# Kernel optimization log

Hardware: AMD Instinct MI355X
Metric: run time of the kernel (lower is better)

The kernel has to match this reference:

```python
import jax, jax.numpy as jnp
import numpy as np

E, H, F, T = 8, 2048, 4096, 16384  # experts, hidden, ffn, total tokens


def setup_inputs() -> dict:
    key = jax.random.key(0)
    k1, k2, k3 = jax.random.split(key, 3)
    std = 1.0 / np.sqrt(H)
    x = jax.random.normal(k1, (T, H), dtype=jnp.float32)
    # trunc_normal_(std=std) ~ normal * std for reference purposes
    w_gate_up = jax.random.normal(k2, (E, 2 * F, H), dtype=jnp.float32) * std
    w_down = jax.random.normal(k3, (E, H, F), dtype=jnp.float32) * std
    # tokens are pre-sorted by expert; uniform routing: T//E tokens per expert
    tokens_per_expert = jnp.full((E,), T // E, dtype=jnp.int64)
    return {"x": x, "w_gate_up": w_gate_up, "w_down": w_down,
            "tokens_per_expert": tokens_per_expert}


def reference(x, w_gate_up, w_down, tokens_per_expert):
    # x: [T, H] sorted by expert; uniform tokens_per_expert => grouped GEMM
    # is a batched GEMM over the expert axis (same math as the per-expert
    # sequential fallback: gate_up = xi @ w_gate_up[i].T, etc.).
    e = w_gate_up.shape[0]
    f = w_down.shape[2]
    xe = x.reshape(e, -1, x.shape[-1])                     # [E, T/E, H]
    gate_up = jnp.einsum('eth,efh->etf', xe, w_gate_up)    # [E, T/E, 2F]
    gate, up = gate_up[..., :f], gate_up[..., f:]
    hidden = jax.nn.silu(gate) * up                        # [E, T/E, F]
    out = jnp.einsum('etf,ehf->eth', hidden, w_down)       # [E, T/E, H]
    return out.reshape(x.shape)
```

## Files before the change

kernel.cpp:

```cpp
#include <hip/hip_runtime.h>
#include <stdint.h>

typedef unsigned short u16;
typedef unsigned int u32;
typedef short bf16x8 __attribute__((ext_vector_type(8)));
typedef float f32x4 __attribute__((ext_vector_type(4)));

#define E_ 8
#define H_ 2048
#define F_ 4096
#define T_ 16384
#define TE_ 2048

#define WAITV(n) asm volatile("s_waitcnt vmcnt(" #n ")" ::: "memory")
#define BARF                       \
  do {                             \
    asm volatile("" ::: "memory"); \
    __builtin_amdgcn_s_barrier();  \
    asm volatile("" ::: "memory"); \
  } while (0)

__device__ __forceinline__ u16 f2bf(float f) {
  u32 u = __builtin_bit_cast(u32, f);
  u32 r = (u + 0x7FFFu + ((u >> 16) & 1u)) >> 16;
  return (u16)r;
}

__device__ __forceinline__ void gload16(const u16* g, u16* l) {
  __builtin_amdgcn_global_load_lds(
      (__attribute__((address_space(1))) void*)g,
      (__attribute__((address_space(3))) void*)l, 16, 0, 0);
}

__device__ __forceinline__ void mfma_b(f32x4& acc, bf16x8 a, bf16x8 b) {
  asm volatile("v_mfma_f32_16x16x32_bf16 %0, %1, %2, %0"
               : "+v"(acc)
               : "v"(a), "v"(b));
}


__global__ __launch_bounds__(256) void cvt3_kernel(
    const float* __restrict__ s0, const float* __restrict__ s1,
    const float* __restrict__ s2, u16* __restrict__ dst, long n0, long n1,
    long n2) {
  long i = (long)blockIdx.x * blockDim.x + threadIdx.x;
  long stride = (long)gridDim.x * blockDim.x;
  const long ntot = n0 + n1 + n2;
  uint2* d4 = (uint2*)dst;
  for (; i < ntot; i += stride) {
    const float4* s4;
    long j;
    if (i < n0) {
      s4 = (const float4*)s0;
      j = i;
    } else if (i < n0 + n1) {
      s4 = (const float4*)s1;
      j = i - n0;
    } else {
      s4 = (const float4*)s2;
      j = i - n0 - n1;
    }
    float4 v = s4[j];
    uint2 o;
    o.x = (u32)f2bf(v.x) | ((u32)f2bf(v.y) << 16);
    o.y = (u32)f2bf(v.z) | ((u32)f2bf(v.w) << 16);
    d4[i] = o;
  }
}


__global__ __launch_bounds__(256, 2) void gemm1_silu(
    const u16* __restrict__ Xb, const u16* __restrict__ Wgu,
    u16* __restrict__ Hid, long sX, long sW, long sH) {
  const int z = blockIdx.z;
  Xb += (long)z * sX;
  Wgu += (long)z * sW;
  Hid += (long)z * sH;

  const int bx = blockIdx.x;
  const int by = blockIdx.y;
  const int tid = threadIdx.x;
  const int w = tid >> 6;
  const int lane = tid & 63;
  const int wr = w >> 1, wc = w & 1;
  const int fr = lane & 15, q = lane >> 4, l7 = lane & 7;

  __shared__ __attribute__((aligned(16))) u16 lds[2 * 16384];

  const int srow8 = lane >> 3;
  const int sgran = (lane & 7) ^ (lane >> 3);
  const u16* gA = Xb + (size_t)(by * 128 + srow8) * H_ + sgran * 8;
  const u16* gBg = Wgu + (size_t)(bx * 64 + srow8) * H_ + sgran * 8;
  const u16* gBu = gBg + (size_t)F_ * H_;

  auto stage = [&](int t, int buf) {
    u16* L = lds + buf * 16384;
    const int ko = t * 64;
#pragma unroll
    for (int i = 0; i < 4; ++i) {
      const int c = i * 4 + w;
      gload16(gA + (size_t)(c * 8) * H_ + ko, L + c * 512 + lane * 8);
    }
#pragma unroll
    for (int i = 0; i < 2; ++i) {
      const int c = i * 4 + w;
      gload16(gBg + (size_t)(c * 8) * H_ + ko, L + 8192 + c * 512 + lane * 8);
      gload16(gBu + (size_t)(c * 8) * H_ + ko, L + 12288 + c * 512 + lane * 8);
    }
  };

  f32x4 accG[4][2] = {};
  f32x4 accU[4][2] = {};

  auto comp = [&](int buf) {
    const u16* L = lds + buf * 16384;
#pragma unroll
    for (int ks = 0; ks < 2; ++ks) {
      const int seg = (((ks << 2) + q) ^ l7) << 3;
      bf16x8 a[4], bg[2], bu[2];
#pragma unroll
      for (int mi = 0; mi < 4; ++mi)
        a[mi] = *(const bf16x8*)&L[(wr * 64 + mi * 16 + fr) * 64 + seg];
#pragma unroll
      for (int ni = 0; ni < 2; ++ni) {
        bg[ni] = *(const bf16x8*)&L[8192 + (wc * 32 + ni * 16 + fr) * 64 + seg];
        bu[ni] =
            *(const bf16x8*)&L[12288 + (wc * 32 + ni * 16 + fr) * 64 + seg];
      }
      __builtin_amdgcn_s_setprio(1);
#pragma unroll
      for (int mi = 0; mi < 4; ++mi)
#pragma unroll
        for (int ni = 0; ni < 2; ++ni) {
          mfma_b(accG[mi][ni], a[mi], bg[ni]);
          mfma_b(accU[mi][ni], a[mi], bu[ni]);
        }
      __builtin_amdgcn_s_setprio(0);
    }
  };

  const int NT = H_ / 64;
  stage(0, 0);
  stage(1, 1);
  for (int t = 0; t < NT - 1; ++t) {
    WAITV(8);
    BARF;
    comp(t & 1);
    BARF;
    if (t + 2 < NT) stage(t + 2, t & 1);
  }
  WAITV(0);
  BARF;
  comp((NT - 1) & 1);

  const int row0 = by * 128 + wr * 64 + q * 4;
  const int col0 = bx * 64 + wc * 32 + fr;
#pragma unroll
  for (int mi = 0; mi < 4; ++mi)
#pragma unroll
    for (int ni = 0; ni < 2; ++ni)
#pragma unroll
      for (int j = 0; j < 4; ++j) {
        float g = accG[mi][ni][j];
        float u = accU[mi][ni][j];
        float h = (g / (1.f + __expf(-g))) * u;
        Hid[(size_t)(row0 + mi * 16 + j) * F_ + col0 + ni * 16] = f2bf(h);
      }
}


__global__ __launch_bounds__(512) void gemm2_down(const u16* __restrict__ Hd,
                                                  const u16* __restrict__ Wd,
                                                  float* __restrict__ Out,
                                                  long sH, long sW, long sO) {
  const int z = blockIdx.z;
  Hd += (long)z * sH;
  Wd += (long)z * sW;
  Out += (long)z * sO;

  const int bx = blockIdx.x;
  const int by = blockIdx.y;
  const int tid = threadIdx.x;
  const int w = tid >> 6;
  const int lane = tid & 63;
  const int wr = w >> 1, wc = w & 1;

  __shared__ __attribute__((aligned(16))) u16 lds[3 * 24576];

  const int srow = (w << 3) + (lane >> 3);
  const int scol = (((lane & 7) ^ (lane >> 3)) << 3);
  const u16* gA = Hd + (size_t)((by << 8) + srow) * F_ + scol;
  const u16* gB = Wd + (size_t)((bx << 7) + srow) * F_ + scol;

  auto stage = [&](int t, int buf) {
    u16* L = &lds[buf * 24576];
    const int ko = t << 6;
    const int wb = w << 3;
#pragma unroll
    for (int i = 0; i < 4; ++i)
      gload16(gA + (size_t)(i * 64) * F_ + ko, &L[((i << 6) + wb) << 6]);
#pragma unroll
    for (int i = 0; i < 2; ++i)
      gload16(gB + (size_t)(i * 64) * F_ + ko,
              &L[16384 + (((i << 6) + wb) << 6)]);
  };

  f32x4 acc[4][4] = {};
  const int fr = lane & 15, q = lane >> 4, l7 = lane & 7;

  auto comp = [&](int buf) {
    const u16* L = &lds[buf * 24576];
    bf16x8 a[4][2], b[4][2];
#pragma unroll
    for (int ni = 0; ni < 4; ++ni)
#pragma unroll
      for (int ks = 0; ks < 2; ++ks) {
        int r = (wc << 6) + (ni << 4) + fr;
        b[ni][ks] =
            *(const bf16x8*)&L[16384 + (r << 6) + ((((ks << 2) + q) ^ l7) << 3)];
      }
#pragma unroll
    for (int mi = 0; mi < 4; ++mi)
#pragma unroll
      for (int ks = 0; ks < 2; ++ks) {
        int r = (wr << 6) + (mi << 4) + fr;
        a[mi][ks] = *(const bf16x8*)&L[(r << 6) + ((((ks << 2) + q) ^ l7) << 3)];
      }
    __builtin_amdgcn_s_setprio(1);
#pragma unroll
    for (int mi = 0; mi < 4; ++mi)
#pragma unroll
      for (int ni = 0; ni < 4; ++ni)
#pragma unroll
        for (int ks = 0; ks < 2; ++ks)
          mfma_b(acc[mi][ni], a[mi][ks], b[ni][ks]);
    __builtin_amdgcn_s_setprio(0);
  };

  const int NT = F_ / 64;
  stage(0, 0);
  stage(1, 1);
  int b0 = 0, b1 = 1, b2 = 2;
  for (int t = 0; t < NT - 2; ++t) {
    stage(t + 2, b2);
    WAITV(12);
    BARF;
    comp(b0);
    BARF;
    int tmp = b0; b0 = b1; b1 = b2; b2 = tmp;
  }
  WAITV(6); BARF;
  comp(b0);
  BARF;
  WAITV(0); BARF;
  comp(b1);

  const int row0 = (by << 8) + (wr << 6) + (q << 2);
  const int col0 = (bx << 7) + (wc << 6) + fr;
#pragma unroll
  for (int mi = 0; mi < 4; ++mi)
#pragma unroll
    for (int ni = 0; ni < 4; ++ni)
#pragma unroll
      for (int j = 0; j < 4; ++j)
        Out[(size_t)(row0 + (mi << 4) + j) * H_ + col0 + (ni << 4)] =
            acc[mi][ni][j];
}


extern "C" void kernel_launch(void* const* d_in, const int* in_sizes, int n_in,
                              void* d_out, int out_size, void* d_ws,
                              size_t ws_size, hipStream_t stream) {
  (void)in_sizes;
  (void)n_in;
  (void)out_size;
  const float* x = (const float*)d_in[0];
  const float* wgu = (const float*)d_in[1];
  const float* wdn = (const float*)d_in[2];
  float* out = (float*)d_out;
  u16* ws = (u16*)d_ws;

  const size_t xbN = (size_t)T_ * H_;
  const size_t wguN = (size_t)E_ * 2 * F_ * H_;
  const size_t wdnN = (size_t)E_ * H_ * F_;
  const size_t hidN = (size_t)T_ * F_;
  const size_t fullBytes = (xbN + wguN + wdnN + hidN) * 2;

  dim3 cblk(256), g1blk(256), g2blk(512);

  if (ws_size >= fullBytes) {
    u16* xb = ws;
    u16* wgub = xb + xbN;
    u16* wdnb = wgub + wguN;
    u16* hid = wdnb + wdnN;
    cvt3_kernel<<<4096, cblk, 0, stream>>>(x, wgu, wdn, ws, (long)(xbN / 4),
                                           (long)(wguN / 4), (long)(wdnN / 4));
    gemm1_silu<<<dim3(F_ / 64, TE_ / 128, E_), g1blk, 0, stream>>>(
        xb, wgub, hid, (long)TE_ * H_, (long)2 * F_ * H_, (long)TE_ * F_);
    gemm2_down<<<dim3(H_ / 128, TE_ / 256, E_), g2blk, 0, stream>>>(
        hid, wdnb, out, (long)TE_ * F_, (long)H_ * F_, (long)TE_ * H_);
  } else {
    u16* xb = ws;
    u16* wgub = xb + (size_t)TE_ * H_;
    u16* wdnb = wgub + (size_t)2 * F_ * H_;
    u16* hid = wdnb + (size_t)H_ * F_;
    for (int e = 0; e < E_; ++e) {
      cvt3_kernel<<<2048, cblk, 0, stream>>>(
          x + (size_t)e * TE_ * H_, wgu + (size_t)e * 2 * F_ * H_,
          wdn + (size_t)e * H_ * F_, ws, (long)((size_t)TE_ * H_ / 4),
          (long)((size_t)2 * F_ * H_ / 4), (long)((size_t)H_ * F_ / 4));
      gemm1_silu<<<dim3(F_ / 64, TE_ / 128, 1), g1blk, 0, stream>>>(xb, wgub,
                                                                    hid, 0, 0,
                                                                    0);
      gemm2_down<<<dim3(H_ / 128, TE_ / 256, 1), g2blk, 0, stream>>>(
          hid, wdnb, out + (size_t)e * TE_ * H_, 0, 0, 0);
    }
  }
}
```

Before: 1.097 ms.

## Retile down-projection GEMM to 128x128 with double buffering; split conversion kernel

New measurement: 1.075 ms, median of 2. Within noise of the previous version (-2.0%).

```diff
diff --git a/kernel.cpp b/kernel.cpp
--- a/kernel.cpp
+++ b/kernel.cpp
@@ -39,28 +39,15 @@
 }
 
 
-__global__ __launch_bounds__(256) void cvt3_kernel(
-    const float* __restrict__ s0, const float* __restrict__ s1,
-    const float* __restrict__ s2, u16* __restrict__ dst, long n0, long n1,
-    long n2) {
+__global__ __launch_bounds__(256) void cvt_kernel(const float* __restrict__ src,
+                                                  u16* __restrict__ dst,
+                                                  long n4) {
   long i = (long)blockIdx.x * blockDim.x + threadIdx.x;
   long stride = (long)gridDim.x * blockDim.x;
-  const long ntot = n0 + n1 + n2;
+  const float4* s4 = (const float4*)src;
   uint2* d4 = (uint2*)dst;
-  for (; i < ntot; i += stride) {
-    const float4* s4;
-    long j;
-    if (i < n0) {
-      s4 = (const float4*)s0;
-      j = i;
-    } else if (i < n0 + n1) {
-      s4 = (const float4*)s1;
-      j = i - n0;
-    } else {
-      s4 = (const float4*)s2;
-      j = i - n0 - n1;
-    }
-    float4 v = s4[j];
+  for (; i < n4; i += stride) {
+    float4 v = s4[i];
     uint2 o;
     o.x = (u32)f2bf(v.x) | ((u32)f2bf(v.y) << 16);
     o.y = (u32)f2bf(v.z) | ((u32)f2bf(v.w) << 16);
@@ -169,10 +156,9 @@
 }
 
 
-__global__ __launch_bounds__(512) void gemm2_down(const u16* __restrict__ Hd,
-                                                  const u16* __restrict__ Wd,
-                                                  float* __restrict__ Out,
-                                                  long sH, long sW, long sO) {
+__global__ __launch_bounds__(256, 2) void gemm2_down(
+    const u16* __restrict__ Hd, const u16* __restrict__ Wd,
+    float* __restrict__ Out, long sH, long sW, long sO) {
   const int z = blockIdx.z;
   Hd += (long)z * sH;
   Wd += (long)z * sW;
@@ -184,86 +170,72 @@
   const int w = tid >> 6;
   const int lane = tid & 63;
   const int wr = w >> 1, wc = w & 1;
-
-  __shared__ __attribute__((aligned(16))) u16 lds[3 * 24576];
-
-  const int srow = (w << 3) + (lane >> 3);
-  const int scol = (((lane & 7) ^ (lane >> 3)) << 3);
-  const u16* gA = Hd + (size_t)((by << 8) + srow) * F_ + scol;
-  const u16* gB = Wd + (size_t)((bx << 7) + srow) * F_ + scol;
+  const int fr = lane & 15, q = lane >> 4, l7 = lane & 7;
+
+  __shared__ __attribute__((aligned(16))) u16 lds[2 * 16384];
+
+  const int srow8 = lane >> 3;
+  const int sgran = (lane & 7) ^ (lane >> 3);
+  const u16* gA = Hd + (size_t)(by * 128 + srow8) * F_ + sgran * 8;
+  const u16* gB = Wd + (size_t)(bx * 128 + srow8) * F_ + sgran * 8;
 
   auto stage = [&](int t, int buf) {
-    u16* L = &lds[buf * 24576];
-    const int ko = t << 6;
-    const int wb = w << 3;
-#pragma unroll
-    for (int i = 0; i < 4; ++i)
-      gload16(gA + (size_t)(i * 64) * F_ + ko, &L[((i << 6) + wb) << 6]);
-#pragma unroll
-    for (int i = 0; i < 2; ++i)
-      gload16(gB + (size_t)(i * 64) * F_ + ko,
-              &L[16384 + (((i << 6) + wb) << 6)]);
+    u16* L = lds + buf * 16384;
+    const int ko = t * 64;
+#pragma unroll
+    for (int i = 0; i < 4; ++i) {
+      const int c = i * 4 + w;
+      gload16(gA + (size_t)(c * 8) * F_ + ko, L + c * 512 + lane * 8);
+      gload16(gB + (size_t)(c * 8) * F_ + ko, L + 8192 + c * 512 + lane * 8);
+    }
   };
 
   f32x4 acc[4][4] = {};
-  const int fr = lane & 15, q = lane >> 4, l7 = lane & 7;
 
   auto comp = [&](int buf) {
-    const u16* L = &lds[buf * 24576];
-    bf16x8 a[4][2], b[4][2];
-#pragma unroll
-    for (int ni = 0; ni < 4; ++ni)
-#pragma unroll
-      for (int ks = 0; ks < 2; ++ks) {
-        int r = (wc << 6) + (ni << 4) + fr;
-        b[ni][ks] =
-            *(const bf16x8*)&L[16384 + (r << 6) + ((((ks << 2) + q) ^ l7) << 3)];
-      }
-#pragma unroll
-    for (int mi = 0; mi < 4; ++mi)
-#pragma unroll
-      for (int ks = 0; ks < 2; ++ks) {
-        int r = (wr << 6) + (mi << 4) + fr;
-        a[mi][ks] = *(const bf16x8*)&L[(r << 6) + ((((ks << 2) + q) ^ l7) << 3)];
-      }
-    __builtin_amdgcn_s_setprio(1);
-#pragma unroll
-    for (int mi = 0; mi < 4; ++mi)
+    const u16* L = lds + buf * 16384;
+#pragma unroll
+    for (int ks = 0; ks < 2; ++ks) {
+      const int seg = (((ks << 2) + q) ^ l7) << 3;
+      bf16x8 a[4], b[4];
+#pragma unroll
+      for (int mi = 0; mi < 4; ++mi)
+        a[mi] = *(const bf16x8*)&L[(wr * 64 + mi * 16 + fr) * 64 + seg];
 #pragma unroll
       for (int ni = 0; ni < 4; ++ni)
-#pragma unroll
-        for (int ks = 0; ks < 2; ++ks)
-          mfma_b(acc[mi][ni], a[mi][ks], b[ni][ks]);
-    __builtin_amdgcn_s_setprio(0);
+        b[ni] = *(const bf16x8*)&L[8192 + (wc * 64 + ni * 16 + fr) * 64 + seg];
+      __builtin_amdgcn_s_setprio(1);
+#pragma unroll
+      for (int mi = 0; mi < 4; ++mi)
+#pragma unroll
+        for (int ni = 0; ni < 4; ++ni) mfma_b(acc[mi][ni], a[mi], b[ni]);
+      __builtin_amdgcn_s_setprio(0);
+    }
   };
 
   const int NT = F_ / 64;
   stage(0, 0);
   stage(1, 1);
-  int b0 = 0, b1 = 1, b2 = 2;
-  for (int t = 0; t < NT - 2; ++t) {
-    stage(t + 2, b2);
-    WAITV(12);
-    BARF;
-    comp(b0);
-    BARF;
-    int tmp = b0; b0 = b1; b1 = b2; b2 = tmp;
-  }
-  WAITV(6); BARF;
-  comp(b0);
+  for (int t = 0; t < NT - 1; ++t) {
+    WAITV(8);
+    BARF;
+    comp(t & 1);
+    BARF;
+    if (t + 2 < NT) stage(t + 2, t & 1);
+  }
+  WAITV(0);
   BARF;
-  WAITV(0); BARF;
-  comp(b1);
-
-  const int row0 = (by << 8) + (wr << 6) + (q << 2);
-  const int col0 = (bx << 7) + (wc << 6) + fr;
+  comp((NT - 1) & 1);
+
+  const int row0 = by * 128 + wr * 64 + q * 4;
+  const int col0 = bx * 128 + wc * 64 + fr;
 #pragma unroll
   for (int mi = 0; mi < 4; ++mi)
 #pragma unroll
     for (int ni = 0; ni < 4; ++ni)
 #pragma unroll
       for (int j = 0; j < 4; ++j)
-        Out[(size_t)(row0 + (mi << 4) + j) * H_ + col0 + (ni << 4)] =
+        Out[(size_t)(row0 + mi * 16 + j) * H_ + col0 + ni * 16] =
             acc[mi][ni][j];
 }
 
@@ -286,18 +258,19 @@
   const size_t hidN = (size_t)T_ * F_;
   const size_t fullBytes = (xbN + wguN + wdnN + hidN) * 2;
 
-  dim3 cblk(256), g1blk(256), g2blk(512);
+  dim3 cblk(256), gblk(256);
 
   if (ws_size >= fullBytes) {
     u16* xb = ws;
     u16* wgub = xb + xbN;
     u16* wdnb = wgub + wguN;
     u16* hid = wdnb + wdnN;
-    cvt3_kernel<<<4096, cblk, 0, stream>>>(x, wgu, wdn, ws, (long)(xbN / 4),
-                                           (long)(wguN / 4), (long)(wdnN / 4));
-    gemm1_silu<<<dim3(F_ / 64, TE_ / 128, E_), g1blk, 0, stream>>>(
+    cvt_kernel<<<2048, cblk, 0, stream>>>(x, xb, (long)(xbN / 4));
+    cvt_kernel<<<4096, cblk, 0, stream>>>(wgu, wgub, (long)(wguN / 4));
+    cvt_kernel<<<4096, cblk, 0, stream>>>(wdn, wdnb, (long)(wdnN / 4));
+    gemm1_silu<<<dim3(F_ / 64, TE_ / 128, E_), gblk, 0, stream>>>(
         xb, wgub, hid, (long)TE_ * H_, (long)2 * F_ * H_, (long)TE_ * F_);
-    gemm2_down<<<dim3(H_ / 128, TE_ / 256, E_), g2blk, 0, stream>>>(
+    gemm2_down<<<dim3(H_ / 128, TE_ / 128, E_), gblk, 0, stream>>>(
         hid, wdnb, out, (long)TE_ * F_, (long)H_ * F_, (long)TE_ * H_);
   } else {
     u16* xb = ws;
@@ -305,14 +278,16 @@
     u16* wdnb = wgub + (size_t)2 * F_ * H_;
     u16* hid = wdnb + (size_t)H_ * F_;
     for (int e = 0; e < E_; ++e) {
-      cvt3_kernel<<<2048, cblk, 0, stream>>>(
-          x + (size_t)e * TE_ * H_, wgu + (size_t)e * 2 * F_ * H_,
-          wdn + (size_t)e * H_ * F_, ws, (long)((size_t)TE_ * H_ / 4),
-          (long)((size_t)2 * F_ * H_ / 4), (long)((size_t)H_ * F_ / 4));
-      gemm1_silu<<<dim3(F_ / 64, TE_ / 128, 1), g1blk, 0, stream>>>(xb, wgub,
-                                                                    hid, 0, 0,
-                                                                    0);
-      gemm2_down<<<dim3(H_ / 128, TE_ / 256, 1), g2blk, 0, stream>>>(
+      cvt_kernel<<<1024, cblk, 0, stream>>>(x + (size_t)e * TE_ * H_, xb,
+                                            (long)((size_t)TE_ * H_ / 4));
+      cvt_kernel<<<2048, cblk, 0, stream>>>(wgu + (size_t)e * 2 * F_ * H_, wgub,
+                                            (long)((size_t)2 * F_ * H_ / 4));
+      cvt_kernel<<<2048, cblk, 0, stream>>>(wdn + (size_t)e * H_ * F_, wdnb,
+                                            (long)((size_t)H_ * F_ / 4));
+      gemm1_silu<<<dim3(F_ / 64, TE_ / 128, 1), gblk, 0, stream>>>(xb, wgub,
+                                                                   hid, 0, 0,
+                                                                   0);
+      gemm2_down<<<dim3(H_ / 128, TE_ / 128, 1), gblk, 0, stream>>>(
           hid, wdnb, out + (size_t)e * TE_ * H_, 0, 0, 0);
     }
   }
```
